# Optimization experiments

Measured on AMD Instinct MI355X. Metric: run time of the kernel, lower is better.

The kernel has to match this reference:

```python
import jax, jax.numpy as jnp
import numpy as np

N_NODES = 50000
N_EDGES = 600000
D = 128
THETA = (0.5, -1.0, 0.5)  # len(theta) must be 3 to match learnable_diag[3, in_feats]


def setup_inputs() -> dict:
    key = jax.random.key(0)
    k1, k2, k3, k4, k5 = jax.random.split(key, 5)
    feat = jax.random.normal(k1, (N_NODES, D), dtype=jnp.float32)
    edge_index = jax.random.randint(k2, (2, N_EDGES), 0, N_NODES)  # [src; dst]
    # learnable_diag = torch.rand(3, in_feats)
    diag = jax.random.uniform(k3, (3, D), dtype=jnp.float32)
    # nn.Linear(out_feats, out_feats) with xavier_uniform weight, zero bias
    limit = float(np.sqrt(6.0 / (D + D)))
    W = jax.random.uniform(k4, (D, D), dtype=jnp.float32, minval=-limit, maxval=limit)
    b = jnp.zeros((D,), dtype=jnp.float32)
    return {"feat": feat, "edge_index": edge_index, "diag": diag, "W": W, "b": b}


def reference(feat, edge_index, diag, W, b):
    src, dst = edge_index[0], edge_index[1]
    n = feat.shape[0]
    # in_degrees: count of incoming edges per node
    deg = jax.ops.segment_sum(jnp.ones_like(dst, dtype=feat.dtype), dst, num_segments=n)
    d_invsqrt = jnp.clip(deg, 1.0, None) ** -0.5  # [N]
    d_invsqrt = d_invsqrt[:, None]  # [N,1]

    h = (THETA[0] * feat) * diag[0]
    h = h @ W.T + b  # nn.Linear

    for k in range(1, len(THETA)):
        # unnLaplacian: feat - (A @ (feat * Dinv)) * Dinv * diag[k]
        msg = feat * d_invsqrt  # [N,D]
        agg = jax.ops.segment_sum(msg[src], dst, num_segments=n)  # SpMM: copy_u + sum
        feat = feat - agg * d_invsqrt * diag[k]
        h = h + THETA[k] * feat
    return h
```

## Files before the change

kernel.cpp:

```cpp
#include <hip/hip_runtime.h>

#define NN 50000
#define NE 600000
#define D  128
#define NBLK 196
#define BCAP 64

typedef __attribute__((ext_vector_type(8))) short bf16x8;
typedef __attribute__((ext_vector_type(4))) float floatx4;
typedef __attribute__((ext_vector_type(2))) float f32x2;

__device__ __forceinline__ unsigned short bf16_rne(float f) {
    union { float f; unsigned u; } v; v.f = f;
    unsigned r = v.u + 0x7FFFu + ((v.u >> 16) & 1u);
    return (unsigned short)(r >> 16);
}
__device__ __forceinline__ unsigned pack2(float a, float b) {
    return (unsigned)bf16_rne(a) | ((unsigned)bf16_rne(b) << 16);
}

__global__ __launch_bounds__(256) void prep_kernel(const float* __restrict__ W,
                                                   const float* __restrict__ diag,
                                                   unsigned short* __restrict__ Wb,
                                                   int* __restrict__ deg_i,
                                                   unsigned int* __restrict__ zrow0,
                                                   unsigned int* __restrict__ zrow1) {
    int g = blockIdx.x * 256 + threadIdx.x;
    if (g < NN) deg_i[g] = 0;
    if (g < 16384) {
        int j = g & 127;
        Wb[g] = bf16_rne(0.5f * diag[j] * W[g]);
    }
    if (g < 64) { zrow0[g] = 0u; zrow1[g] = 0u; }
}

__global__ __launch_bounds__(256) void bucket_fill_kernel(const int* __restrict__ src,
                                                          const int* __restrict__ dst,
                                                          int* __restrict__ deg_i,
                                                          int* __restrict__ buck) {
    const int e = (blockIdx.x * 256 + threadIdx.x) * 4;
    if (e >= NE) return;
    const int4 d4 = *(const int4*)(dst + e);
    const int4 s4 = *(const int4*)(src + e);
    int c;
    c = atomicAdd(&deg_i[d4.x], 1); if (c < BCAP) buck[(d4.x << 6) + c] = s4.x;
    c = atomicAdd(&deg_i[d4.y], 1); if (c < BCAP) buck[(d4.y << 6) + c] = s4.y;
    c = atomicAdd(&deg_i[d4.z], 1); if (c < BCAP) buck[(d4.z << 6) + c] = s4.z;
    c = atomicAdd(&deg_i[d4.w], 1); if (c < BCAP) buck[(d4.w << 6) + c] = s4.w;
}

__global__ __launch_bounds__(256) void gemm_mfma_kernel(const float* __restrict__ feat,
                                                        const unsigned short* __restrict__ Wb,
                                                        const float* __restrict__ b,
                                                        const int* __restrict__ deg_i,
                                                        unsigned short* __restrict__ featb_s,
                                                        float* __restrict__ out) {
    const int wv   = threadIdx.x >> 6;
    const int lane = threadIdx.x & 63;
    const int r16  = lane & 15;
    const int quad = lane >> 4;
    const int m0   = blockIdx.x * 64 + wv * 16;

    const int mrow = m0 + r16;
    const int mc   = (mrow < NN) ? mrow : (NN - 1);
    const float* arow = feat + (size_t)mc * D + quad * 8;
    const float di = rsqrtf(fmaxf((float)deg_i[mc], 1.0f));

    bf16x8 afrag[4];
    #pragma unroll
    for (int kc = 0; kc < 4; ++kc) {
        const float4 f0 = *(const float4*)(arow + kc * 32);
        const float4 f1 = *(const float4*)(arow + kc * 32 + 4);
        bf16x8 a;
        a[0] = (short)bf16_rne(f0.x); a[1] = (short)bf16_rne(f0.y);
        a[2] = (short)bf16_rne(f0.z); a[3] = (short)bf16_rne(f0.w);
        a[4] = (short)bf16_rne(f1.x); a[5] = (short)bf16_rne(f1.y);
        a[6] = (short)bf16_rne(f1.z); a[7] = (short)bf16_rne(f1.w);
        afrag[kc] = a;
        if (mrow < NN) {
            uint4 st;
            st.x = pack2(f0.x * di, f0.y * di);
            st.y = pack2(f0.z * di, f0.w * di);
            st.z = pack2(f1.x * di, f1.y * di);
            st.w = pack2(f1.z * di, f1.w * di);
            *(uint4*)(featb_s + (size_t)mc * D + quad * 8 + kc * 32) = st;
        }
    }

    floatx4 acc[8];
    #pragma unroll
    for (int nt = 0; nt < 8; ++nt) acc[nt] = (floatx4)(0.0f);

    #pragma unroll
    for (int nt = 0; nt < 8; ++nt) {
        const unsigned short* brow = Wb + (size_t)(nt * 16 + r16) * D + quad * 8;
        #pragma unroll
        for (int kc = 0; kc < 4; ++kc) {
            const bf16x8 bfrag = *(const bf16x8*)(brow + kc * 32);
            acc[nt] = __builtin_amdgcn_mfma_f32_16x16x32_bf16(afrag[kc], bfrag, acc[nt], 0, 0, 0);
        }
    }

    #pragma unroll
    for (int nt = 0; nt < 8; ++nt) {
        const int d = nt * 16 + r16;
        const float bd = b[d];
        #pragma unroll
        for (int r = 0; r < 4; ++r) {
            const int i = m0 + quad * 4 + r;
            if (i < NN) out[(size_t)i * D + d] = acc[nt][r] + bd;
        }
    }
}

__device__ __forceinline__ floatx4 gather_acc(const unsigned short* __restrict__ rows,
                                              const int* __restrict__ buck,
                                              int node, int bcnt, int lane) {
    const int half = lane >> 5;
    const unsigned lane_b = (unsigned)((lane & 31) << 3);
    int s = (lane < bcnt) ? buck[(node << 6) + lane] : NN;
    f32x2 a01 = (f32x2)(0.0f);
    f32x2 a23 = (f32x2)(0.0f);
    const int cnt4 = (bcnt + 3) & ~3;
    for (int k = 0; k < cnt4; k += 4) {
        #pragma unroll
        for (int u = 0; u < 2; ++u) {
            int ss = __shfl(s, k + 2 * u + half);
            const uint2 pv = *(const uint2*)((const char*)rows +
                                (((unsigned)ss << 8) | lane_b));
            f32x2 lo0, lo1;
            lo0.x = __uint_as_float(pv.x << 16);
            lo0.y = __uint_as_float(pv.x & 0xFFFF0000u);
            lo1.x = __uint_as_float(pv.y << 16);
            lo1.y = __uint_as_float(pv.y & 0xFFFF0000u);
            a01 += lo0;
            a23 += lo1;
        }
    }
    floatx4 r;
    r[0] = a01.x; r[1] = a01.y; r[2] = a23.x; r[3] = a23.y;
    #pragma unroll
    for (int i = 0; i < 4; ++i) r[i] += __shfl_xor(r[i], 32);
    return r;
}

__global__ __launch_bounds__(256) void gather1_kernel(const unsigned short* __restrict__ featb_s,
                                                      const int* __restrict__ buck,
                                                      const int* __restrict__ deg_i,
                                                      const float* __restrict__ diag,
                                                      const float* __restrict__ feat0,
                                                      unsigned short* __restrict__ feat1s) {
    const int node = blockIdx.x * 4 + (threadIdx.x >> 6);
    const int lane = threadIdx.x & 63;
    const int dg   = deg_i[node];
    floatx4 acc = gather_acc(featb_s, buck, node, min(dg, BCAP), lane);
    if (lane < 32) {
        const int c0 = lane << 2;
        const float di = rsqrtf(fmaxf((float)dg, 1.0f));
        const float4 bs = *(const float4*)(feat0 + (size_t)node * D + c0);
        const float4 dg4 = *(const float4*)(diag + D + c0);
        const float r0 = (bs.x - acc[0] * di * dg4.x) * di;
        const float r1 = (bs.y - acc[1] * di * dg4.y) * di;
        const float r2 = (bs.z - acc[2] * di * dg4.z) * di;
        const float r3 = (bs.w - acc[3] * di * dg4.w) * di;
        uint2 st; st.x = pack2(r0, r1); st.y = pack2(r2, r3);
        *(uint2*)((char*)feat1s + ((size_t)node << 8) + (lane << 3)) = st;
    }
}

__global__ __launch_bounds__(256) void gather2_kernel(const unsigned short* __restrict__ feat1s,
                                                      const int* __restrict__ buck,
                                                      const int* __restrict__ deg_i,
                                                      const float* __restrict__ diag,
                                                      float* __restrict__ outp) {
    const int node = blockIdx.x * 4 + (threadIdx.x >> 6);
    const int lane = threadIdx.x & 63;
    const int dg   = deg_i[node];
    floatx4 acc = gather_acc(feat1s, buck, node, min(dg, BCAP), lane);
    if (lane < 32) {
        const int c0 = lane << 2;
        const float dc = fmaxf((float)dg, 1.0f);
        const float di = rsqrtf(dc);
        const float rd = sqrtf(dc);
        const uint2 bp = *(const uint2*)((const char*)feat1s + ((size_t)node << 8) + (lane << 3));
        const float b0 = __uint_as_float(bp.x << 16) * rd;
        const float b1 = __uint_as_float(bp.x & 0xFFFF0000u) * rd;
        const float b2 = __uint_as_float(bp.y << 16) * rd;
        const float b3 = __uint_as_float(bp.y & 0xFFFF0000u) * rd;
        const float4 dg4 = *(const float4*)(diag + 2 * D + c0);
        float4 cur = *(float4*)(outp + (size_t)node * D + c0);
        cur.x -= 0.5f * (b0 + acc[0] * di * dg4.x);
        cur.y -= 0.5f * (b1 + acc[1] * di * dg4.y);
        cur.z -= 0.5f * (b2 + acc[2] * di * dg4.z);
        cur.w -= 0.5f * (b3 + acc[3] * di * dg4.w);
        *(float4*)(outp + (size_t)node * D + c0) = cur;
    }
}

extern "C" void kernel_launch(void* const* d_in, const int* in_sizes, int n_in,
                              void* d_out, int out_size, void* d_ws, size_t ws_size,
                              hipStream_t stream) {
    const float* feat = (const float*)d_in[0];
    const int*   eidx = (const int*)d_in[1];
    const float* diag = (const float*)d_in[2];
    const float* W    = (const float*)d_in[3];
    const float* b    = (const float*)d_in[4];
    float* out = (float*)d_out;

    const int* src = eidx;
    const int* dst = eidx + NE;

    unsigned short* featb_s = (unsigned short*)d_ws;
    unsigned short* feat1s  = featb_s + (size_t)(NN + 1) * D;
    int*   buck    = (int*)(feat1s + (size_t)(NN + 1) * D);
    int*   deg_i   = buck + (size_t)NN * BCAP;
    unsigned short* Wb = (unsigned short*)(deg_i + NN);

    unsigned int* zr0 = (unsigned int*)(featb_s + (size_t)NN * D);
    unsigned int* zr1 = (unsigned int*)(feat1s + (size_t)NN * D);

    prep_kernel<<<NBLK, 256, 0, stream>>>(W, diag, Wb, deg_i, zr0, zr1);

    bucket_fill_kernel<<<(NE / 4 + 255) / 256, 256, 0, stream>>>(src, dst, deg_i, buck);

    gemm_mfma_kernel<<<(NN + 63) / 64, 256, 0, stream>>>(feat, Wb, b, deg_i, featb_s, out);

    gather1_kernel<<<NN / 4, 256, 0, stream>>>(featb_s, buck, deg_i, diag, feat, feat1s);
    gather2_kernel<<<NN / 4, 256, 0, stream>>>(feat1s, buck, deg_i, diag, out);
}
```

Baseline: 198.1 us.

## Split gather feature tables into column blocks with 16-bit neighbor buckets

The bf16 feature tables are stored as four 32-column slices. Each gather pass is launched over all slices, so every wave gathers a 64-byte segment per neighbour, with eight neighbours handled per load, and reduces partial sums through shuffles. The aim is a per-slice working set small enough to stay in cache during the random gathers. Neighbour indices are stored as unsigned short to halve bucket traffic, and nontemporal loads and stores are added on streaming arrays. The 16-bit indices cannot represent node IDs of 65536 or more. That is safe for 50000 nodes but tightly ties the code to this size. The bucket lists are now read four times, and only 8 lanes do the epilogue work.

```diff
diff --git a/kernel.cpp b/kernel.cpp
--- a/kernel.cpp
+++ b/kernel.cpp
@@ -5,10 +5,13 @@
 #define D  128
 #define NBLK 196
 #define BCAP 64
+#define NTI 12500
+#define SLICE_U ((NN + 1) * 32)
 
 typedef __attribute__((ext_vector_type(8))) short bf16x8;
 typedef __attribute__((ext_vector_type(4))) float floatx4;
 typedef __attribute__((ext_vector_type(2))) float f32x2;
+typedef __attribute__((ext_vector_type(2))) unsigned int u32x2;
 
 __device__ __forceinline__ unsigned short bf16_rne(float f) {
     union { float f; unsigned u; } v; v.f = f;
@@ -23,37 +26,38 @@
                                                    const float* __restrict__ diag,
                                                    unsigned short* __restrict__ Wb,
                                                    int* __restrict__ deg_i,
-                                                   unsigned int* __restrict__ zrow0,
-                                                   unsigned int* __restrict__ zrow1) {
+                                                   unsigned int* __restrict__ z0,
+                                                   unsigned int* __restrict__ z1) {
     int g = blockIdx.x * 256 + threadIdx.x;
     if (g < NN) deg_i[g] = 0;
-    if (g < 16384) {
-        int j = g & 127;
-        Wb[g] = bf16_rne(0.5f * diag[j] * W[g]);
-    }
-    if (g < 64) { zrow0[g] = 0u; zrow1[g] = 0u; }
+    if (g < 16384) Wb[g] = bf16_rne(0.5f * diag[g & 127] * W[g]);
+    if (g < 64) {
+        int cb = g >> 4, w = g & 15;
+        int idx = cb * ((NN + 1) * 16) + NN * 16 + w;
+        z0[idx] = 0u; z1[idx] = 0u;
+    }
 }
 
 __global__ __launch_bounds__(256) void bucket_fill_kernel(const int* __restrict__ src,
                                                           const int* __restrict__ dst,
                                                           int* __restrict__ deg_i,
-                                                          int* __restrict__ buck) {
+                                                          unsigned short* __restrict__ buck) {
     const int e = (blockIdx.x * 256 + threadIdx.x) * 4;
     if (e >= NE) return;
     const int4 d4 = *(const int4*)(dst + e);
     const int4 s4 = *(const int4*)(src + e);
     int c;
-    c = atomicAdd(&deg_i[d4.x], 1); if (c < BCAP) buck[(d4.x << 6) + c] = s4.x;
-    c = atomicAdd(&deg_i[d4.y], 1); if (c < BCAP) buck[(d4.y << 6) + c] = s4.y;
-    c = atomicAdd(&deg_i[d4.z], 1); if (c < BCAP) buck[(d4.z << 6) + c] = s4.z;
-    c = atomicAdd(&deg_i[d4.w], 1); if (c < BCAP) buck[(d4.w << 6) + c] = s4.w;
+    c = atomicAdd(&deg_i[d4.x], 1); if (c < BCAP) buck[(d4.x << 6) + c] = (unsigned short)s4.x;
+    c = atomicAdd(&deg_i[d4.y], 1); if (c < BCAP) buck[(d4.y << 6) + c] = (unsigned short)s4.y;
+    c = atomicAdd(&deg_i[d4.z], 1); if (c < BCAP) buck[(d4.z << 6) + c] = (unsigned short)s4.z;
+    c = atomicAdd(&deg_i[d4.w], 1); if (c < BCAP) buck[(d4.w << 6) + c] = (unsigned short)s4.w;
 }
 
 __global__ __launch_bounds__(256) void gemm_mfma_kernel(const float* __restrict__ feat,
                                                         const unsigned short* __restrict__ Wb,
                                                         const float* __restrict__ b,
                                                         const int* __restrict__ deg_i,
-                                                        unsigned short* __restrict__ featb_s,
+                                                        unsigned short* __restrict__ featbCB,
                                                         float* __restrict__ out) {
     const int wv   = threadIdx.x >> 6;
     const int lane = threadIdx.x & 63;
@@ -69,21 +73,21 @@
     bf16x8 afrag[4];
     #pragma unroll
     for (int kc = 0; kc < 4; ++kc) {
-        const float4 f0 = *(const float4*)(arow + kc * 32);
-        const float4 f1 = *(const float4*)(arow + kc * 32 + 4);
+        const floatx4 f0 = __builtin_nontemporal_load((const floatx4*)(arow + kc * 32));
+        const floatx4 f1 = __builtin_nontemporal_load((const floatx4*)(arow + kc * 32 + 4));
         bf16x8 a;
-        a[0] = (short)bf16_rne(f0.x); a[1] = (short)bf16_rne(f0.y);
-        a[2] = (short)bf16_rne(f0.z); a[3] = (short)bf16_rne(f0.w);
-        a[4] = (short)bf16_rne(f1.x); a[5] = (short)bf16_rne(f1.y);
-        a[6] = (short)bf16_rne(f1.z); a[7] = (short)bf16_rne(f1.w);
+        a[0] = (short)bf16_rne(f0[0]); a[1] = (short)bf16_rne(f0[1]);
+        a[2] = (short)bf16_rne(f0[2]); a[3] = (short)bf16_rne(f0[3]);
+        a[4] = (short)bf16_rne(f1[0]); a[5] = (short)bf16_rne(f1[1]);
+        a[6] = (short)bf16_rne(f1[2]); a[7] = (short)bf16_rne(f1[3]);
         afrag[kc] = a;
         if (mrow < NN) {
             uint4 st;
-            st.x = pack2(f0.x * di, f0.y * di);
-            st.y = pack2(f0.z * di, f0.w * di);
-            st.z = pack2(f1.x * di, f1.y * di);
-            st.w = pack2(f1.z * di, f1.w * di);
-            *(uint4*)(featb_s + (size_t)mc * D + quad * 8 + kc * 32) = st;
+            st.x = pack2(f0[0] * di, f0[1] * di);
+            st.y = pack2(f0[2] * di, f0[3] * di);
+            st.z = pack2(f1[0] * di, f1[1] * di);
+            st.w = pack2(f1[2] * di, f1[3] * di);
+            *(uint4*)(featbCB + (size_t)kc * SLICE_U + (size_t)mc * 32 + quad * 8) = st;
         }
     }
 
@@ -108,92 +112,97 @@
         #pragma unroll
         for (int r = 0; r < 4; ++r) {
             const int i = m0 + quad * 4 + r;
-            if (i < NN) out[(size_t)i * D + d] = acc[nt][r] + bd;
+            if (i < NN) __builtin_nontemporal_store(acc[nt][r] + bd, out + (size_t)i * D + d);
         }
     }
 }
 
-__device__ __forceinline__ floatx4 gather_acc(const unsigned short* __restrict__ rows,
-                                              const int* __restrict__ buck,
-                                              int node, int bcnt, int lane) {
-    const int half = lane >> 5;
-    const unsigned lane_b = (unsigned)((lane & 31) << 3);
-    int s = (lane < bcnt) ? buck[(node << 6) + lane] : NN;
+__device__ __forceinline__ floatx4 gather_cb(const unsigned short* __restrict__ rows,
+                                             const unsigned short* __restrict__ buck,
+                                             int node, int bcnt, int lane) {
+    const int slot = lane >> 3;
+    const unsigned lane_b = (unsigned)((lane & 7) << 3);
+    int s = (lane < bcnt) ? (int)__builtin_nontemporal_load(&buck[(node << 6) + lane]) : NN;
     f32x2 a01 = (f32x2)(0.0f);
     f32x2 a23 = (f32x2)(0.0f);
-    const int cnt4 = (bcnt + 3) & ~3;
-    for (int k = 0; k < cnt4; k += 4) {
-        #pragma unroll
-        for (int u = 0; u < 2; ++u) {
-            int ss = __shfl(s, k + 2 * u + half);
-            const uint2 pv = *(const uint2*)((const char*)rows +
-                                (((unsigned)ss << 8) | lane_b));
-            f32x2 lo0, lo1;
-            lo0.x = __uint_as_float(pv.x << 16);
-            lo0.y = __uint_as_float(pv.x & 0xFFFF0000u);
-            lo1.x = __uint_as_float(pv.y << 16);
-            lo1.y = __uint_as_float(pv.y & 0xFFFF0000u);
-            a01 += lo0;
-            a23 += lo1;
-        }
-    }
-    floatx4 r;
-    r[0] = a01.x; r[1] = a01.y; r[2] = a23.x; r[3] = a23.y;
-    #pragma unroll
-    for (int i = 0; i < 4; ++i) r[i] += __shfl_xor(r[i], 32);
+    const int cnt8 = (bcnt + 7) & ~7;
+    for (int k = 0; k < cnt8; k += 8) {
+        int ss = __shfl(s, k + slot);
+        const u32x2 pv = *(const u32x2*)((const char*)rows + (((unsigned)ss << 6) | lane_b));
+        f32x2 lo0, lo1;
+        lo0.x = __uint_as_float(pv.x << 16);
+        lo0.y = __uint_as_float(pv.x & 0xFFFF0000u);
+        lo1.x = __uint_as_float(pv.y << 16);
+        lo1.y = __uint_as_float(pv.y & 0xFFFF0000u);
+        a01 += lo0;
+        a23 += lo1;
+    }
+    floatx4 r; r[0] = a01.x; r[1] = a01.y; r[2] = a23.x; r[3] = a23.y;
+    #pragma unroll
+    for (int m = 8; m <= 32; m <<= 1) {
+        r[0] += __shfl_xor(r[0], m);
+        r[1] += __shfl_xor(r[1], m);
+        r[2] += __shfl_xor(r[2], m);
+        r[3] += __shfl_xor(r[3], m);
+    }
     return r;
 }
 
-__global__ __launch_bounds__(256) void gather1_kernel(const unsigned short* __restrict__ featb_s,
-                                                      const int* __restrict__ buck,
+__global__ __launch_bounds__(256) void gather1_kernel(const unsigned short* __restrict__ featbCB,
+                                                      const unsigned short* __restrict__ buck,
                                                       const int* __restrict__ deg_i,
                                                       const float* __restrict__ diag,
                                                       const float* __restrict__ feat0,
-                                                      unsigned short* __restrict__ feat1s) {
-    const int node = blockIdx.x * 4 + (threadIdx.x >> 6);
+                                                      unsigned short* __restrict__ feat1CB) {
+    const int cb   = blockIdx.x / NTI;
+    const int node = (blockIdx.x - cb * NTI) * 4 + (threadIdx.x >> 6);
     const int lane = threadIdx.x & 63;
     const int dg   = deg_i[node];
-    floatx4 acc = gather_acc(featb_s, buck, node, min(dg, BCAP), lane);
-    if (lane < 32) {
-        const int c0 = lane << 2;
+    const unsigned short* rows = featbCB + (size_t)cb * SLICE_U;
+    floatx4 acc = gather_cb(rows, buck, node, min(dg, BCAP), lane);
+    if (lane < 8) {
+        const int c0 = cb * 32 + lane * 4;
         const float di = rsqrtf(fmaxf((float)dg, 1.0f));
-        const float4 bs = *(const float4*)(feat0 + (size_t)node * D + c0);
-        const float4 dg4 = *(const float4*)(diag + D + c0);
-        const float r0 = (bs.x - acc[0] * di * dg4.x) * di;
-        const float r1 = (bs.y - acc[1] * di * dg4.y) * di;
-        const float r2 = (bs.z - acc[2] * di * dg4.z) * di;
-        const float r3 = (bs.w - acc[3] * di * dg4.w) * di;
-        uint2 st; st.x = pack2(r0, r1); st.y = pack2(r2, r3);
-        *(uint2*)((char*)feat1s + ((size_t)node << 8) + (lane << 3)) = st;
-    }
-}
-
-__global__ __launch_bounds__(256) void gather2_kernel(const unsigned short* __restrict__ feat1s,
-                                                      const int* __restrict__ buck,
+        const floatx4 bs = __builtin_nontemporal_load((const floatx4*)(feat0 + (size_t)node * D + c0));
+        const floatx4 dgv = *(const floatx4*)(diag + D + c0);
+        const float r0 = (bs[0] - acc[0] * di * dgv[0]) * di;
+        const float r1 = (bs[1] - acc[1] * di * dgv[1]) * di;
+        const float r2 = (bs[2] - acc[2] * di * dgv[2]) * di;
+        const float r3 = (bs[3] - acc[3] * di * dgv[3]) * di;
+        u32x2 st; st.x = pack2(r0, r1); st.y = pack2(r2, r3);
+        *(u32x2*)(feat1CB + (size_t)cb * SLICE_U + (size_t)node * 32 + lane * 4) = st;
+    }
+}
+
+__global__ __launch_bounds__(256) void gather2_kernel(const unsigned short* __restrict__ feat1CB,
+                                                      const unsigned short* __restrict__ buck,
                                                       const int* __restrict__ deg_i,
                                                       const float* __restrict__ diag,
                                                       float* __restrict__ outp) {
-    const int node = blockIdx.x * 4 + (threadIdx.x >> 6);
+    const int cb   = blockIdx.x / NTI;
+    const int node = (blockIdx.x - cb * NTI) * 4 + (threadIdx.x >> 6);
     const int lane = threadIdx.x & 63;
     const int dg   = deg_i[node];
-    floatx4 acc = gather_acc(feat1s, buck, node, min(dg, BCAP), lane);
-    if (lane < 32) {
-        const int c0 = lane << 2;
+    const unsigned short* rows = feat1CB + (size_t)cb * SLICE_U;
+    floatx4 acc = gather_cb(rows, buck, node, min(dg, BCAP), lane);
+    if (lane < 8) {
+        const int c0 = cb * 32 + lane * 4;
         const float dc = fmaxf((float)dg, 1.0f);
         const float di = rsqrtf(dc);
         const float rd = sqrtf(dc);
-        const uint2 bp = *(const uint2*)((const char*)feat1s + ((size_t)node << 8) + (lane << 3));
+        const u32x2 bp = *(const u32x2*)(feat1CB + (size_t)cb * SLICE_U + (size_t)node * 32 + lane * 4);
         const float b0 = __uint_as_float(bp.x << 16) * rd;
         const float b1 = __uint_as_float(bp.x & 0xFFFF0000u) * rd;
         const float b2 = __uint_as_float(bp.y << 16) * rd;
         const float b3 = __uint_as_float(bp.y & 0xFFFF0000u) * rd;
-        const float4 dg4 = *(const float4*)(diag + 2 * D + c0);
-        float4 cur = *(float4*)(outp + (size_t)node * D + c0);
-        cur.x -= 0.5f * (b0 + acc[0] * di * dg4.x);
-        cur.y -= 0.5f * (b1 + acc[1] * di * dg4.y);
-        cur.z -= 0.5f * (b2 + acc[2] * di * dg4.z);
-        cur.w -= 0.5f * (b3 + acc[3] * di * dg4.w);
-        *(float4*)(outp + (size_t)node * D + c0) = cur;
+        const floatx4 dgv = *(const floatx4*)(diag + 2 * D + c0);
+        float* op = outp + (size_t)node * D + c0;
+        floatx4 cur = __builtin_nontemporal_load((const floatx4*)op);
+        cur[0] -= 0.5f * (b0 + acc[0] * di * dgv[0]);
+        cur[1] -= 0.5f * (b1 + acc[1] * di * dgv[1]);
+        cur[2] -= 0.5f * (b2 + acc[2] * di * dgv[2]);
+        cur[3] -= 0.5f * (b3 + acc[3] * di * dgv[3]);
+        __builtin_nontemporal_store(cur, (floatx4*)op);
     }
 }
 
@@ -210,21 +219,19 @@
     const int* src = eidx;
     const int* dst = eidx + NE;
 
-    unsigned short* featb_s = (unsigned short*)d_ws;
-    unsigned short* feat1s  = featb_s + (size_t)(NN + 1) * D;
-    int*   buck    = (int*)(feat1s + (size_t)(NN + 1) * D);
-    int*   deg_i   = buck + (size_t)NN * BCAP;
+    unsigned short* featbCB = (unsigned short*)d_ws;
+    unsigned short* feat1CB = featbCB + 4 * (size_t)SLICE_U;
+    unsigned short* buck16  = feat1CB + 4 * (size_t)SLICE_U;
+    int*   deg_i   = (int*)(buck16 + (size_t)NN * BCAP);
     unsigned short* Wb = (unsigned short*)(deg_i + NN);
 
-    unsigned int* zr0 = (unsigned int*)(featb_s + (size_t)NN * D);
-    unsigned int* zr1 = (unsigned int*)(feat1s + (size_t)NN * D);
-
-    prep_kernel<<<NBLK, 256, 0, stream>>>(W, diag, Wb, deg_i, zr0, zr1);
-
-    bucket_fill_kernel<<<(NE / 4 + 255) / 256, 256, 0, stream>>>(src, dst, deg_i, buck);
-
-    gemm_mfma_kernel<<<(NN + 63) / 64, 256, 0, stream>>>(feat, Wb, b, deg_i, featb_s, out);
-
-    gather1_kernel<<<NN / 4, 256, 0, stream>>>(featb_s, buck, deg_i, diag, feat, feat1s);
-    gather2_kernel<<<NN / 4, 256, 0, stream>>>(feat1s, buck, deg_i, diag, out);
-}
+    prep_kernel<<<NBLK, 256, 0, stream>>>(W, diag, Wb, deg_i,
+                                          (unsigned int*)featbCB, (unsigned int*)feat1CB);
+
+    bucket_fill_kernel<<<(NE / 4 + 255) / 256, 256, 0, stream>>>(src, dst, deg_i, buck16);
+
+    gemm_mfma_kernel<<<(NN + 63) / 64, 256, 0, stream>>>(feat, Wb, b, deg_i, featbCB, out);
+
+    gather1_kernel<<<4 * NTI, 256, 0, stream>>>(featbCB, buck16, deg_i, diag, feat, feat1CB);
+    gather2_kernel<<<4 * NTI, 256, 0, stream>>>(feat1CB, buck16, deg_i, diag, out);
+}
```

New measurement: 300.9 us. +51.9%, slower.
